# Optimization experiments

Hardware: AMD Instinct MI355X
Metric: run time of the kernel (lower is better)

Reference implementation:

```python
import jax, jax.numpy as jnp
import numpy as np

B, S, HID, NH = 2, 2048, 2048, 16
HD = HID // NH          # head_size = 128
ROPE_THETA = 10000.0
SCALING = HD ** -0.5


def setup_inputs() -> dict:
    key = jax.random.key(0)
    ks = jax.random.split(key, 8)
    std = 1.0 / np.sqrt(HID)
    inp = {
        "hidden_states": jax.random.normal(ks[0], (B, S, HID), jnp.float32),
        "positions": jnp.broadcast_to(jnp.arange(S, dtype=jnp.int32), (B, S)),
        "wq": jax.random.normal(ks[1], (HID, HID), jnp.float32) * std,
        "bq": jax.random.normal(ks[2], (HID,), jnp.float32) * 0.02,
        "wk": jax.random.normal(ks[3], (HID, HID), jnp.float32) * std,
        "bk": jax.random.normal(ks[4], (HID,), jnp.float32) * 0.02,
        "wv": jax.random.normal(ks[5], (HID, HID), jnp.float32) * std,
        "bv": jax.random.normal(ks[6], (HID,), jnp.float32) * 0.02,
        "wc": jax.random.normal(ks[7], (HID, HID), jnp.float32) * std,
    }
    return inp


def _rope_neox(x, positions):
    # x: [B, S, NH, HD]; positions: [B, S] int
    half = HD // 2
    inv_freq = 1.0 / (ROPE_THETA ** (jnp.arange(half, dtype=jnp.float32) * (2.0 / HD)))
    freqs = positions.astype(jnp.float32)[..., None] * inv_freq      # [B,S,half]
    cos = jnp.cos(freqs)[:, :, None, :]                               # [B,S,1,half]
    sin = jnp.sin(freqs)[:, :, None, :]
    x1, x2 = x[..., :half], x[..., half:]
    return jnp.concatenate([x1 * cos - x2 * sin, x2 * cos + x1 * sin], axis=-1)


def reference(hidden_states, positions, wq, bq, wk, bk, wv, bv, wc):
    # fused QKV projections
    q = hidden_states @ wq + bq
    k = hidden_states @ wk + bk
    v = hidden_states @ wv + bv
    q = q.reshape(B, S, NH, HD)
    k = k.reshape(B, S, NH, HD)
    v = v.reshape(B, S, NH, HD)
    # neox-style rotary embedding over full head dim
    q = _rope_neox(q, positions)
    k = _rope_neox(k, positions)
    # causal self-attention (prefill path of RadixAttention)
    scores = jnp.einsum("bqhd,bkhd->bhqk", q, k) * SCALING
    causal = jnp.tril(jnp.ones((S, S), dtype=bool))
    scores = jnp.where(causal, scores, jnp.finfo(scores.dtype).min)
    probs = jax.nn.softmax(scores, axis=-1)
    attn = jnp.einsum("bhqk,bkhd->bqhd", probs, v).reshape(B, S, HID)
    # output projection (no bias)
    return attn @ wc
```

## Files before the change

kernel.cpp:

```cpp
#include <hip/hip_runtime.h>
#include <stdint.h>

constexpr int Bsz = 2;
constexpr int Ssz = 2048;
constexpr int Hid = 2048;
constexpr int NHd = 16;
constexpr int Hd  = 128;
constexpr int Mrows = Bsz * Ssz;

typedef __bf16 bf16;
typedef __bf16 bf16x8 __attribute__((ext_vector_type(8)));
typedef __bf16 bf16x4 __attribute__((ext_vector_type(4)));
typedef float  f32x4  __attribute__((ext_vector_type(4)));
typedef float  f32x16 __attribute__((ext_vector_type(16)));

__device__ __forceinline__ void gload_lds16(const bf16* g, bf16* l) {
  __builtin_amdgcn_global_load_lds((const __attribute__((address_space(1))) void*)g,
                                   (__attribute__((address_space(3))) void*)l, 16, 0, 0);
}

__device__ __forceinline__ uint32_t pkbf(bf16 a, bf16 b) {
  union { bf16 hh[2]; uint32_t u; } x;
  x.hh[0] = a; x.hh[1] = b;
  return x.u;
}
__device__ __forceinline__ uint32_t pkff(float a, float b) {
  return pkbf((bf16)a, (bf16)b);
}

__global__ void k_cvt(const float* __restrict__ in, bf16* __restrict__ out, int n4) {
  int i = blockIdx.x * blockDim.x + threadIdx.x;
  if (i >= n4) return;
  float4 v = ((const float4*)in)[i];
  bf16x4 o = { (bf16)v.x, (bf16)v.y, (bf16)v.z, (bf16)v.w };
  ((bf16x4*)out)[i] = o;
}

__global__ void k_wtrans(const float* __restrict__ w0, const float* __restrict__ w1,
                         const float* __restrict__ w2, const float* __restrict__ w3,
                         bf16* __restrict__ out) {
  __shared__ float tile[32][33];
  int z = blockIdx.z;
  const float* w = (z == 0) ? w0 : (z == 1) ? w1 : (z == 2) ? w2 : w3;
  bf16* o = out + (size_t)z * Hid * Hid;
  int n0 = blockIdx.x * 32, k0 = blockIdx.y * 32;
  int tx = threadIdx.x, ty = threadIdx.y;
#pragma unroll
  for (int i = 0; i < 4; i++)
    tile[ty + i * 8][tx] = w[(size_t)(k0 + ty + i * 8) * Hid + n0 + tx];
  __syncthreads();
#pragma unroll
  for (int i = 0; i < 4; i++)
    o[(size_t)(n0 + ty + i * 8) * Hid + k0 + tx] = (bf16)tile[tx][ty + i * 8];
}

__device__ __forceinline__ bf16x8 rdfrag(const bf16* t, int row, int kslot) {
  return *(const bf16x8*)((const char*)t + row * 128 + (((kslot ^ (row & 7)) & 7) << 4));
}

__device__ __forceinline__ void stage_half(const bf16* g, bf16* l, int w, int lane) {
  const int rsub = lane >> 3;
  const int slot = (lane & 7) ^ rsub;
#pragma unroll
  for (int j = 0; j < 2; ++j) {
    const int blk = w * 2 + j;
    gload_lds16(g + (size_t)(blk * 8 + rsub) * Hid + slot * 8, l + blk * 512);
  }
}

#define PH_SYNC()                                      \
  __builtin_amdgcn_s_barrier();                        \
  asm volatile("s_waitcnt lgkmcnt(0)" ::: "memory");   \
  __builtin_amdgcn_sched_barrier(0);

template <int MODE, int CHM, int CHN>
__global__ __launch_bounds__(512, 1) void k_gemm(const bf16* __restrict__ A,
                                                 const bf16* __restrict__ Bt,
                                                 const float* __restrict__ biasq,
                                                 const float* __restrict__ biask,
                                                 const float* __restrict__ biasv,
                                                 bf16* __restrict__ Qo, bf16* __restrict__ Ko,
                                                 bf16* __restrict__ Vo, float* __restrict__ Fo) {
  constexpr int KK = Hid;
  constexpr int NT = KK / 64;
  __shared__ bf16 smA[2][256 * 64];
  __shared__ bf16 smB[2][128 * 64];
  const int hw = blockIdx.y * gridDim.x + blockIdx.x;
  const int chunk = hw & 7, within = hw >> 3;
  const int chunk_rows = gridDim.y / CHM;
  const int cr = chunk % chunk_rows, cc = chunk / chunk_rows;
  const int mt = cr * CHM + within % CHM;
  const int nt = cc * CHN + within / CHM;
  const int m0 = mt * 256, n0 = nt * 128;
  const int tid = threadIdx.x, lane = tid & 63, w = tid >> 6;
  const int wm = w >> 2, wn = w & 3;
  const int frow = lane & 15, a4 = lane >> 4;
  const bf16* Ag = A + (size_t)m0 * KK;
  const bf16* Bg = Bt + (size_t)n0 * KK;
  f32x4 acc[8][2] = {};
  stage_half(Ag,                    smA[0],            w, lane);
  stage_half(Ag + (size_t)128 * KK, smA[0] + 128 * 64, w, lane);
  stage_half(Bg,                    smB[0],            w, lane);
  stage_half(Bg + 64,               smB[1],            w, lane);
  asm volatile("s_waitcnt vmcnt(2)" ::: "memory");
  __builtin_amdgcn_sched_barrier(0);
  __builtin_amdgcn_s_barrier();
  for (int it = 0; it < NT / 2; ++it) {
    const int base = 2 * it;
    const bool has2 = (base + 2) < NT;
    const bool has3 = (base + 3) < NT;
    bf16x8 af[4][2], bfr[2][2];
#pragma unroll
    for (int f = 0; f < 4; ++f)
#pragma unroll
      for (int kk = 0; kk < 2; ++kk)
        af[f][kk] = rdfrag(smA[0], wm * 128 + f * 16 + frow, kk * 4 + a4);
#pragma unroll
    for (int nf = 0; nf < 2; ++nf)
#pragma unroll
      for (int kk = 0; kk < 2; ++kk)
        bfr[nf][kk] = rdfrag(smB[0], wn * 32 + nf * 16 + frow, kk * 4 + a4);
    {
      const size_t kA1 = (size_t)(base + 1) * 64;
      stage_half(Ag + kA1,                    smA[1],            w, lane);
      stage_half(Ag + (size_t)128 * KK + kA1, smA[1] + 128 * 64, w, lane);
    }
    PH_SYNC();
    __builtin_amdgcn_s_setprio(1);
#pragma unroll
    for (int f = 0; f < 4; ++f)
#pragma unroll
      for (int nf = 0; nf < 2; ++nf)
#pragma unroll
        for (int kk = 0; kk < 2; ++kk)
          acc[f][nf] = __builtin_amdgcn_mfma_f32_16x16x32_bf16(
              af[f][kk], bfr[nf][kk], acc[f][nf], 0, 0, 0);
    __builtin_amdgcn_s_setprio(0);
    __builtin_amdgcn_s_barrier();
#pragma unroll
    for (int f = 0; f < 4; ++f)
#pragma unroll
      for (int kk = 0; kk < 2; ++kk)
        af[f][kk] = rdfrag(smA[0], wm * 128 + (4 + f) * 16 + frow, kk * 4 + a4);
    if (has2) stage_half(Bg + (size_t)(base + 2) * 64, smB[0], w, lane);
    PH_SYNC();
    __builtin_amdgcn_s_setprio(1);
#pragma unroll
    for (int f = 0; f < 4; ++f)
#pragma unroll
      for (int nf = 0; nf < 2; ++nf)
#pragma unroll
        for (int kk = 0; kk < 2; ++kk)
          acc[4 + f][nf] = __builtin_amdgcn_mfma_f32_16x16x32_bf16(
              af[f][kk], bfr[nf][kk], acc[4 + f][nf], 0, 0, 0);
    __builtin_amdgcn_s_setprio(0);
    if (has2) { asm volatile("s_waitcnt vmcnt(2)" ::: "memory"); }
    else      { asm volatile("s_waitcnt vmcnt(0)" ::: "memory"); }
    __builtin_amdgcn_sched_barrier(0);
    __builtin_amdgcn_s_barrier();
#pragma unroll
    for (int f = 0; f < 4; ++f)
#pragma unroll
      for (int kk = 0; kk < 2; ++kk)
        af[f][kk] = rdfrag(smA[1], wm * 128 + f * 16 + frow, kk * 4 + a4);
#pragma unroll
    for (int nf = 0; nf < 2; ++nf)
#pragma unroll
      for (int kk = 0; kk < 2; ++kk)
        bfr[nf][kk] = rdfrag(smB[1], wn * 32 + nf * 16 + frow, kk * 4 + a4);
    if (has2) {
      const size_t kA2 = (size_t)(base + 2) * 64;
      stage_half(Ag + kA2,                    smA[0],            w, lane);
      stage_half(Ag + (size_t)128 * KK + kA2, smA[0] + 128 * 64, w, lane);
    }
    PH_SYNC();
    __builtin_amdgcn_s_setprio(1);
#pragma unroll
    for (int f = 0; f < 4; ++f)
#pragma unroll
      for (int nf = 0; nf < 2; ++nf)
#pragma unroll
        for (int kk = 0; kk < 2; ++kk)
          acc[f][nf] = __builtin_amdgcn_mfma_f32_16x16x32_bf16(
              af[f][kk], bfr[nf][kk], acc[f][nf], 0, 0, 0);
    __builtin_amdgcn_s_setprio(0);
    __builtin_amdgcn_s_barrier();
#pragma unroll
    for (int f = 0; f < 4; ++f)
#pragma unroll
      for (int kk = 0; kk < 2; ++kk)
        af[f][kk] = rdfrag(smA[1], wm * 128 + (4 + f) * 16 + frow, kk * 4 + a4);
    if (has3) stage_half(Bg + (size_t)(base + 3) * 64, smB[1], w, lane);
    PH_SYNC();
    __builtin_amdgcn_s_setprio(1);
#pragma unroll
    for (int f = 0; f < 4; ++f)
#pragma unroll
      for (int nf = 0; nf < 2; ++nf)
#pragma unroll
        for (int kk = 0; kk < 2; ++kk)
          acc[4 + f][nf] = __builtin_amdgcn_mfma_f32_16x16x32_bf16(
              af[f][kk], bfr[nf][kk], acc[4 + f][nf], 0, 0, 0);
    __builtin_amdgcn_s_setprio(0);
    if (has2) {
      if (has3) { asm volatile("s_waitcnt vmcnt(2)" ::: "memory"); }
      else      { asm volatile("s_waitcnt vmcnt(0)" ::: "memory"); }
      __builtin_amdgcn_sched_barrier(0);
    }
    __builtin_amdgcn_s_barrier();
  }
  if (MODE == 0) {
    const int z = n0 >> 11;
    const float* bias = (z == 0) ? biasq : (z == 1) ? biask : biasv;
    bf16* o = (z == 0) ? Qo : (z == 1) ? Ko : Vo;
    const float oscale = (z == 1) ? (float)(0.08838834764831845 * 1.4426950408889634) : 1.0f;
#pragma unroll
    for (int nf = 0; nf < 2; ++nf) {
      const int col = n0 + wn * 32 + nf * 16 + frow;
      const float bb_ = bias[col & 2047];
      const int h = (col >> 7) & 15, hd = col & (Hd - 1);
#pragma unroll
      for (int mf = 0; mf < 8; ++mf) {
#pragma unroll
        for (int r = 0; r < 4; ++r) {
          const int row = m0 + wm * 128 + mf * 16 + a4 * 4 + r;
          const int bb = row >> 11, ss = row & (Ssz - 1);
          o[(((size_t)bb * NHd + h) * Ssz + ss) * Hd + hd] = (bf16)((acc[mf][nf][r] + bb_) * oscale);
        }
      }
    }
  } else {
#pragma unroll
    for (int mf = 0; mf < 8; ++mf)
#pragma unroll
      for (int nf = 0; nf < 2; ++nf) {
        const int col = n0 + wn * 32 + nf * 16 + frow;
#pragma unroll
        for (int r = 0; r < 4; ++r) {
          const int row = m0 + wm * 128 + mf * 16 + a4 * 4 + r;
          Fo[(size_t)row * Hid + col] = acc[mf][nf][r];
        }
      }
  }
}

__global__ void k_rope(bf16* __restrict__ Q, bf16* __restrict__ Kk, const int* __restrict__ pos) {
  const int idx = blockIdx.x * 256 + threadIdx.x;
  const int i = idx & 63;
  const int s = (idx >> 6) & (Ssz - 1);
  const int bh = idx >> 17;
  const int b = bh >> 4;
  const float p = (float)pos[b * Ssz + s];
  const float f = p * exp2f(-(float)i * 0.20762050593046014f);
  float sn, cs;
  sincosf(f, &sn, &cs);
  const size_t base = ((size_t)bh * Ssz + s) * Hd;
  float x1 = (float)Q[base + i], x2 = (float)Q[base + i + 64];
  Q[base + i]      = (bf16)(x1 * cs - x2 * sn);
  Q[base + i + 64] = (bf16)(x2 * cs + x1 * sn);
  x1 = (float)Kk[base + i]; x2 = (float)Kk[base + i + 64];
  Kk[base + i]      = (bf16)(x1 * cs - x2 * sn);
  Kk[base + i + 64] = (bf16)(x2 * cs + x1 * sn);
}

__global__ __launch_bounds__(256, 2) void k_attn(const bf16* __restrict__ Qg,
                                                 const bf16* __restrict__ Kg,
                                                 const bf16* __restrict__ Vg,
                                                 bf16* __restrict__ AO) {
  const int bh = blockIdx.y;
  int qc = blockIdx.x;
  if (bh & 1) qc = 15 - qc;
  const int tid = threadIdx.x, lane = tid & 63, w = tid >> 6;
  const int l31 = lane & 31, h = lane >> 5;
  __shared__ bf16 Ks[2][64 * 128];
  __shared__ bf16 Vt[2][128 * 72];
  const size_t hbase = (size_t)bh * Ssz * Hd;
  const int q0 = qc * 128 + w * 32;
  bf16x8 qf[8];
  {
    const bf16* qp = Qg + hbase + (size_t)(q0 + l31) * Hd + h * 8;
#pragma unroll
    for (int c = 0; c < 8; c++) qf[c] = *(const bf16x8*)(qp + c * 16);
  }
  float m = -1e30f, lsum = 0.f;
  f32x16 o[4] = {};
  const int NT = 2 * (qc + 1);
  const int r4  = (tid >> 4) << 2;
  const int hd0 = (tid & 15) << 3;
  bf16x8 vv[4];
#pragma unroll
  for (int p = 0; p < 4; p++)
    vv[p] = *(const bf16x8*)(Vg + hbase + (size_t)(r4 + p) * Hd + hd0);
  __builtin_amdgcn_sched_barrier(0);
#pragma unroll
  for (int i = 0; i < 4; i++) {
    const int db  = (w * 4 + i) * 1024 + (lane << 4);
    const int row = db >> 8;
    const int cb  = (db & 255) ^ ((row & 7) << 4);
    gload_lds16(Kg + hbase + row * Hd + (cb >> 1), Ks[0] + (w * 4 + i) * 512);
  }
  for (int t = 0; t < NT; ++t) {
    const int kv0 = t * 64;
    const int cur = t & 1;
    asm volatile("s_waitcnt vmcnt(4)" ::: "memory");
#pragma unroll
    for (int j = 0; j < 8; j++) {
      uint2 wv;
      wv.x = pkbf(vv[0][j], vv[1][j]);
      wv.y = pkbf(vv[2][j], vv[3][j]);
      const int hd = hd0 + j;
      const int cb = (r4 * 2) ^ (((hd >> 3) & 7) << 4);
      *(uint2*)((char*)(Vt[cur]) + hd * 144 + cb) = wv;
    }
    const int tn = (t + 1 < NT) ? t + 1 : t;
    const size_t nb = (size_t)tn * 64;
#pragma unroll
    for (int p = 0; p < 4; p++)
      vv[p] = *(const bf16x8*)(Vg + hbase + (nb + r4 + p) * Hd + hd0);
    __builtin_amdgcn_sched_barrier(0);
#pragma unroll
    for (int i = 0; i < 4; i++) {
      const int db  = (w * 4 + i) * 1024 + (lane << 4);
      const int row = db >> 8;
      const int cb  = (db & 255) ^ ((row & 7) << 4);
      gload_lds16(Kg + hbase + (nb + row) * Hd + (cb >> 1), Ks[cur ^ 1] + (w * 4 + i) * 512);
    }
    asm volatile("s_waitcnt vmcnt(8) lgkmcnt(0)" ::: "memory");
    __builtin_amdgcn_sched_barrier(0);
    __builtin_amdgcn_s_barrier();
    if (kv0 <= q0 + 31) {
      const bf16* KsC = Ks[cur];
      const bf16* VtC = Vt[cur];
      f32x16 s0 = {}, s1 = {};
#pragma unroll
      for (int c = 0; c < 8; c++) {
        const int cb = (c * 32 + h * 16) ^ ((l31 & 7) << 4);
        bf16x8 k0 = *(const bf16x8*)((const char*)KsC + l31 * 256 + cb);
        bf16x8 k1 = *(const bf16x8*)((const char*)KsC + (32 + l31) * 256 + cb);
        s0 = __builtin_amdgcn_mfma_f32_32x32x16_bf16(k0, qf[c], s0, 0, 0, 0);
        s1 = __builtin_amdgcn_mfma_f32_32x32x16_bf16(k1, qf[c], s1, 0, 0, 0);
      }
      if (kv0 + 63 > q0) {
        const int qg = q0 + l31;
        const int kb = kv0 + 4 * h;
#pragma unroll
        for (int r = 0; r < 16; r++) {
          const int cr = (r & 3) + 8 * (r >> 2);
          if (kb + cr > qg)      s0[r] = -1e30f;
          if (kb + 32 + cr > qg) s1[r] = -1e30f;
        }
      }
      float tm = s0[0];
#pragma unroll
      for (int r = 1; r < 16; r++) tm = fmaxf(tm, s0[r]);
#pragma unroll
      for (int r = 0; r < 16; r++) tm = fmaxf(tm, s1[r]);
      tm = fmaxf(tm, __shfl_xor(tm, 32));
      if (!__all(tm - m <= 8.0f)) {
        const float mn = fmaxf(m, tm);
        const float rs = exp2f(m - mn);
        m = mn; lsum *= rs;
#pragma unroll
        for (int ct = 0; ct < 4; ct++)
#pragma unroll
          for (int r = 0; r < 16; r++) o[ct][r] *= rs;
      }
      float ps = 0.f;
#pragma unroll
      for (int r = 0; r < 16; r++) { s0[r] = exp2f(s0[r] - m); ps += s0[r]; }
#pragma unroll
      for (int r = 0; r < 16; r++) { s1[r] = exp2f(s1[r] - m); ps += s1[r]; }
      ps += __shfl_xor(ps, 32);
      lsum += ps;
      uint32_t gw[8][2];
#pragma unroll
      for (int g = 0; g < 4; g++) {
        gw[g][0]     = pkff(s0[4 * g], s0[4 * g + 1]);
        gw[g][1]     = pkff(s0[4 * g + 2], s0[4 * g + 3]);
        gw[4 + g][0] = pkff(s1[4 * g], s1[4 * g + 1]);
        gw[4 + g][1] = pkff(s1[4 * g + 2], s1[4 * g + 3]);
      }
#pragma unroll
      for (int kc = 0; kc < 4; kc++) {
        const uint32_t a0 = gw[2 * kc][0], a1 = gw[2 * kc][1];
        const uint32_t b0 = gw[2 * kc + 1][0], b1 = gw[2 * kc + 1][1];
        const uint32_t sd0 = h ? a0 : b0, sd1 = h ? a1 : b1;
        const uint32_t r0 = (uint32_t)__shfl_xor((int)sd0, 32);
        const uint32_t r1 = (uint32_t)__shfl_xor((int)sd1, 32);
        union { uint32_t u[4]; bf16x8 v; } pa;
        pa.u[0] = h ? r0 : a0; pa.u[1] = h ? r1 : a1;
        pa.u[2] = h ? b0 : r0; pa.u[3] = h ? b1 : r1;
#pragma unroll
        for (int ct = 0; ct < 4; ct++) {
          const int row = ct * 32 + l31;
          const int cb = (kc * 32 + h * 16) ^ (((row >> 3) & 7) << 4);
          bf16x8 vf = *(const bf16x8*)((const char*)VtC + row * 144 + cb);
          o[ct] = __builtin_amdgcn_mfma_f32_32x32x16_bf16(pa.v, vf, o[ct], 0, 0, 0);
        }
      }
    }
    __builtin_amdgcn_s_barrier();
  }
  const float linv = 1.0f / lsum;
  float li[16];
#pragma unroll
  for (int r = 0; r < 16; r++)
    li[r] = __shfl(linv, (r & 3) + 8 * (r >> 2) + 4 * h);
  const int b = bh >> 4, hh = bh & 15;
#pragma unroll
  for (int ct = 0; ct < 4; ct++) {
#pragma unroll
    for (int r = 0; r < 16; r++) {
      const int qrow = q0 + (r & 3) + 8 * (r >> 2) + 4 * h;
      AO[((size_t)b * Ssz + qrow) * Hid + hh * Hd + ct * 32 + l31] = (bf16)(o[ct][r] * li[r]);
    }
  }
}

extern "C" void kernel_launch(void* const* d_in, const int* in_sizes, int n_in,
                              void* d_out, int out_size, void* d_ws, size_t ws_size,
                              hipStream_t stream) {
  (void)in_sizes; (void)n_in; (void)out_size; (void)ws_size;
  const float* hidden   = (const float*)d_in[0];
  const int*   positions= (const int*)d_in[1];
  const float* wq = (const float*)d_in[2];
  const float* bq = (const float*)d_in[3];
  const float* wk = (const float*)d_in[4];
  const float* bk = (const float*)d_in[5];
  const float* wv = (const float*)d_in[6];
  const float* bv = (const float*)d_in[7];
  const float* wc = (const float*)d_in[8];
  float* out = (float*)d_out;

  char* ws = (char*)d_ws;
  bf16* WT  = (bf16*)ws;
  bf16* Hbf = (bf16*)(ws + (size_t)4 * Hid * Hid * 2);
  bf16* Qb  = (bf16*)(ws + (size_t)4 * Hid * Hid * 2 + (size_t)Mrows * Hid * 2);
  bf16* Kb  = Qb + (size_t)Mrows * Hid;
  bf16* Vb  = Kb + (size_t)Mrows * Hid;

  k_cvt<<<dim3(Mrows * Hid / 4 / 256), dim3(256), 0, stream>>>(hidden, Hbf, Mrows * Hid / 4);
  k_wtrans<<<dim3(Hid / 32, Hid / 32, 4), dim3(32, 8), 0, stream>>>(wq, wk, wv, wc, WT);
  k_gemm<0, 8, 12><<<dim3(48, 16), dim3(512), 0, stream>>>(
      Hbf, WT, bq, bk, bv, Qb, Kb, Vb, nullptr);
  k_rope<<<dim3(Bsz * NHd * Ssz * 64 / 256), dim3(256), 0, stream>>>(Qb, Kb, positions);
  k_attn<<<dim3(16, Bsz * NHd), dim3(256), 0, stream>>>(Qb, Kb, Vb, Hbf );
  k_gemm<1, 8, 4><<<dim3(16, 16), dim3(512), 0, stream>>>(
      Hbf, WT + (size_t)3 * Hid * Hid, nullptr, nullptr, nullptr,
      nullptr, nullptr, nullptr, out);
}
```

Before: 298.0 us.

## Use 256x192 tiles in a dedicated QKV GEMM kernel

Adds a separate QKV projection kernel with 256x192 output tiles instead of 256x128. The grid shrinks from 768 to 512 blocks, which matches the 256 CUs in exactly two waves and reuses each A tile across more columns. Each wave now holds 48 columns, computed as three 16-wide fragments with a restructured MFMA/staging schedule. The trade-off is more accumulator registers and LDS per block, plus a different barrier pattern that may expose more load latency. The generic GEMM template is reduced to the fp32 output-projection path only.

```diff
diff --git a/kernel.cpp b/kernel.cpp
--- a/kernel.cpp
+++ b/kernel.cpp
@@ -68,19 +68,144 @@
   }
 }
 
+__device__ __forceinline__ void stage_192(const bf16* g, bf16* l, int w, int lane) {
+  const int rsub = lane >> 3;
+  const int slot = (lane & 7) ^ rsub;
+#pragma unroll
+  for (int j = 0; j < 3; ++j) {
+    const int blk = w * 3 + j;
+    gload_lds16(g + (size_t)(blk * 8 + rsub) * Hid + slot * 8, l + blk * 512);
+  }
+}
+
 #define PH_SYNC()                                      \
   __builtin_amdgcn_s_barrier();                        \
   asm volatile("s_waitcnt lgkmcnt(0)" ::: "memory");   \
   __builtin_amdgcn_sched_barrier(0);
 
-template <int MODE, int CHM, int CHN>
+__global__ __launch_bounds__(512, 1) void k_qkv(const bf16* __restrict__ A,
+                                                const bf16* __restrict__ Bt,
+                                                const float* __restrict__ biasq,
+                                                const float* __restrict__ biask,
+                                                const float* __restrict__ biasv,
+                                                bf16* __restrict__ Qo, bf16* __restrict__ Ko,
+                                                bf16* __restrict__ Vo) {
+  constexpr int KK = Hid;
+  constexpr int NT = KK / 64;
+  __shared__ bf16 smA[2][256 * 64];
+  __shared__ bf16 smB[2][192 * 64];
+  const int hw = blockIdx.y * gridDim.x + blockIdx.x;
+  const int chunk = hw & 7, within = hw >> 3;
+  const int cr = chunk & 1, cc = chunk >> 1;
+  const int mt = cr * 8 + (within & 7);
+  const int nt = cc * 8 + (within >> 3);
+  const int m0 = mt * 256, n0 = nt * 192;
+  const int tid = threadIdx.x, lane = tid & 63, w = tid >> 6;
+  const int wm = w >> 2, wn = w & 3;
+  const int frow = lane & 15, a4 = lane >> 4;
+  const bf16* Ag = A + (size_t)m0 * KK;
+  const bf16* Bg = Bt + (size_t)n0 * KK;
+  f32x4 acc[8][3] = {};
+  stage_half(Ag,                    smA[0],            w, lane);
+  stage_half(Ag + (size_t)128 * KK, smA[0] + 128 * 64, w, lane);
+  stage_192 (Bg,                    smB[0],            w, lane);
+  asm volatile("s_waitcnt vmcnt(0)" ::: "memory");
+  __builtin_amdgcn_s_barrier();
+  for (int kt = 0; kt < NT; ++kt) {
+    const bf16* At  = smA[kt & 1];
+    const bf16* Btl = smB[kt & 1];
+    bf16* As2 = smA[(kt + 1) & 1];
+    bf16* Bs2 = smB[(kt + 1) & 1];
+    const bool more = (kt + 1) < NT;
+    const size_t kn = (size_t)(kt + 1) * 64;
+    bf16x8 afA[4][2], afB[4][2], bfr[3][2];
+#pragma unroll
+    for (int f = 0; f < 4; ++f)
+#pragma unroll
+      for (int kk = 0; kk < 2; ++kk)
+        afA[f][kk] = rdfrag(At, wm * 128 + f * 16 + frow, kk * 4 + a4);
+#pragma unroll
+    for (int nf = 0; nf < 3; ++nf)
+#pragma unroll
+      for (int kk = 0; kk < 2; ++kk)
+        bfr[nf][kk] = rdfrag(Btl, wn * 48 + nf * 16 + frow, kk * 4 + a4);
+    if (more) {
+      stage_half(Ag + kn,                    As2,            w, lane);
+      stage_half(Ag + (size_t)128 * KK + kn, As2 + 128 * 64, w, lane);
+    }
+    PH_SYNC();
+    __builtin_amdgcn_s_setprio(1);
+#pragma unroll
+    for (int f = 0; f < 4; ++f)
+#pragma unroll
+      for (int nf = 0; nf < 2; ++nf)
+#pragma unroll
+        for (int kk = 0; kk < 2; ++kk)
+          acc[f][nf] = __builtin_amdgcn_mfma_f32_16x16x32_bf16(
+              afA[f][kk], bfr[nf][kk], acc[f][nf], 0, 0, 0);
+    __builtin_amdgcn_s_setprio(0);
+    __builtin_amdgcn_s_barrier();
+#pragma unroll
+    for (int f = 0; f < 4; ++f)
+#pragma unroll
+      for (int kk = 0; kk < 2; ++kk)
+        afB[f][kk] = rdfrag(At, wm * 128 + 64 + f * 16 + frow, kk * 4 + a4);
+    if (more) stage_192(Bg + kn, Bs2, w, lane);
+    PH_SYNC();
+    __builtin_amdgcn_s_setprio(1);
+#pragma unroll
+    for (int f = 0; f < 4; ++f)
+#pragma unroll
+      for (int nf = 0; nf < 2; ++nf)
+#pragma unroll
+        for (int kk = 0; kk < 2; ++kk)
+          acc[4 + f][nf] = __builtin_amdgcn_mfma_f32_16x16x32_bf16(
+              afB[f][kk], bfr[nf][kk], acc[4 + f][nf], 0, 0, 0);
+    __builtin_amdgcn_s_setprio(0);
+    __builtin_amdgcn_s_barrier();
+    __builtin_amdgcn_s_setprio(1);
+#pragma unroll
+    for (int f = 0; f < 4; ++f)
+#pragma unroll
+      for (int kk = 0; kk < 2; ++kk)
+        acc[f][2] = __builtin_amdgcn_mfma_f32_16x16x32_bf16(
+            afA[f][kk], bfr[2][kk], acc[f][2], 0, 0, 0);
+#pragma unroll
+    for (int f = 0; f < 4; ++f)
+#pragma unroll
+      for (int kk = 0; kk < 2; ++kk)
+        acc[4 + f][2] = __builtin_amdgcn_mfma_f32_16x16x32_bf16(
+            afB[f][kk], bfr[2][kk], acc[4 + f][2], 0, 0, 0);
+    __builtin_amdgcn_s_setprio(0);
+    asm volatile("s_waitcnt vmcnt(0)" ::: "memory");
+    __builtin_amdgcn_sched_barrier(0);
+    __builtin_amdgcn_s_barrier();
+  }
+#pragma unroll
+  for (int nf = 0; nf < 3; ++nf) {
+    const int col = n0 + wn * 48 + nf * 16 + frow;
+    const int z = col >> 11;
+    const float* bias = (z == 0) ? biasq : (z == 1) ? biask : biasv;
+    bf16* o = (z == 0) ? Qo : (z == 1) ? Ko : Vo;
+    const float oscale = (z == 1) ? (float)(0.08838834764831845 * 1.4426950408889634) : 1.0f;
+    const float bb_ = bias[col & 2047];
+    const int h = (col >> 7) & 15, hd = col & (Hd - 1);
+#pragma unroll
+    for (int mf = 0; mf < 8; ++mf) {
+#pragma unroll
+      for (int r = 0; r < 4; ++r) {
+        const int row = m0 + wm * 128 + mf * 16 + a4 * 4 + r;
+        const int bb = row >> 11, ss = row & (Ssz - 1);
+        o[(((size_t)bb * NHd + h) * Ssz + ss) * Hd + hd] = (bf16)((acc[mf][nf][r] + bb_) * oscale);
+      }
+    }
+  }
+}
+
+template <int CHM, int CHN>
 __global__ __launch_bounds__(512, 1) void k_gemm(const bf16* __restrict__ A,
                                                  const bf16* __restrict__ Bt,
-                                                 const float* __restrict__ biasq,
-                                                 const float* __restrict__ biask,
-                                                 const float* __restrict__ biasv,
-                                                 bf16* __restrict__ Qo, bf16* __restrict__ Ko,
-                                                 bf16* __restrict__ Vo, float* __restrict__ Fo) {
+                                                 float* __restrict__ Fo) {
   constexpr int KK = Hid;
   constexpr int NT = KK / 64;
   __shared__ bf16 smA[2][256 * 64];
@@ -209,39 +334,17 @@
     }
     __builtin_amdgcn_s_barrier();
   }
-  if (MODE == 0) {
-    const int z = n0 >> 11;
-    const float* bias = (z == 0) ? biasq : (z == 1) ? biask : biasv;
-    bf16* o = (z == 0) ? Qo : (z == 1) ? Ko : Vo;
-    const float oscale = (z == 1) ? (float)(0.08838834764831845 * 1.4426950408889634) : 1.0f;
+#pragma unroll
+  for (int mf = 0; mf < 8; ++mf)
 #pragma unroll
     for (int nf = 0; nf < 2; ++nf) {
       const int col = n0 + wn * 32 + nf * 16 + frow;
-      const float bb_ = bias[col & 2047];
-      const int h = (col >> 7) & 15, hd = col & (Hd - 1);
-#pragma unroll
-      for (int mf = 0; mf < 8; ++mf) {
-#pragma unroll
-        for (int r = 0; r < 4; ++r) {
-          const int row = m0 + wm * 128 + mf * 16 + a4 * 4 + r;
-          const int bb = row >> 11, ss = row & (Ssz - 1);
-          o[(((size_t)bb * NHd + h) * Ssz + ss) * Hd + hd] = (bf16)((acc[mf][nf][r] + bb_) * oscale);
-        }
-      }
-    }
-  } else {
-#pragma unroll
-    for (int mf = 0; mf < 8; ++mf)
-#pragma unroll
-      for (int nf = 0; nf < 2; ++nf) {
-        const int col = n0 + wn * 32 + nf * 16 + frow;
-#pragma unroll
-        for (int r = 0; r < 4; ++r) {
-          const int row = m0 + wm * 128 + mf * 16 + a4 * 4 + r;
-          Fo[(size_t)row * Hid + col] = acc[mf][nf][r];
-        }
-      }
-  }
+#pragma unroll
+      for (int r = 0; r < 4; ++r) {
+        const int row = m0 + wm * 128 + mf * 16 + a4 * 4 + r;
+        Fo[(size_t)row * Hid + col] = acc[mf][nf][r];
+      }
+    }
 }
 
 __global__ void k_rope(bf16* __restrict__ Q, bf16* __restrict__ Kk, const int* __restrict__ pos) {
@@ -441,11 +544,10 @@
 
   k_cvt<<<dim3(Mrows * Hid / 4 / 256), dim3(256), 0, stream>>>(hidden, Hbf, Mrows * Hid / 4);
   k_wtrans<<<dim3(Hid / 32, Hid / 32, 4), dim3(32, 8), 0, stream>>>(wq, wk, wv, wc, WT);
-  k_gemm<0, 8, 12><<<dim3(48, 16), dim3(512), 0, stream>>>(
-      Hbf, WT, bq, bk, bv, Qb, Kb, Vb, nullptr);
+  k_qkv<<<dim3(32, 16), dim3(512), 0, stream>>>(
+      Hbf, WT, bq, bk, bv, Qb, Kb, Vb);
   k_rope<<<dim3(Bsz * NHd * Ssz * 64 / 256), dim3(256), 0, stream>>>(Qb, Kb, positions);
   k_attn<<<dim3(16, Bsz * NHd), dim3(256), 0, stream>>>(Qb, Kb, Vb, Hbf );
-  k_gemm<1, 8, 4><<<dim3(16, 16), dim3(512), 0, stream>>>(
-      Hbf, WT + (size_t)3 * Hid * Hid, nullptr, nullptr, nullptr,
-      nullptr, nullptr, nullptr, out);
-}
+  k_gemm<8, 4><<<dim3(16, 16), dim3(512), 0, stream>>>(
+      Hbf, WT + (size_t)3 * Hid * Hid, out);
+}
```

After: 282.7 us. 1.05x faster.
